# Kernel optimization log

Measured on AMD Instinct MI355X. Metric: run time of the kernel, lower is better.

Reference implementation:

```python
import jax, jax.numpy as jnp
import numpy as np

# dims matching init_kwargs
B, C, T = 64, 8, 2048
K, DIL = 16, 4            # kernel_size, dilation
MLP = 16                  # mlp_dim
NF = min(MLP, K // 2 + 1) # n_frequencies = 9
FEAT = C * NF * 2         # 144
H1, H2 = 64, 32           # ReLUBlock hidden dims (64 -> 64//2)
EFF = DIL * (K - 1)       # 60
W = T - EFF               # 1988 windows


def setup_inputs() -> dict:
    key = jax.random.key(0)
    ks = jax.random.split(key, 10)
    def lin(k, out_d, in_d):
        kw, kb = jax.random.split(k)
        bound = 1.0 / np.sqrt(in_d)
        w = jax.random.uniform(kw, (out_d, in_d), jnp.float32, -bound, bound)
        b = jax.random.uniform(kb, (out_d,), jnp.float32, -bound, bound)
        return w, b
    x = jax.random.normal(ks[0], (B, C, T), jnp.float32)
    proj_w, proj_b = lin(ks[1], MLP, FEAT)
    w1, b1 = lin(ks[2], H1, MLP)
    w2, b2 = lin(ks[3], H2, H1)
    out_w, out_b = lin(ks[4], 1, H2)
    agg_w = jax.random.normal(ks[5], (W,), jnp.float32) * 0.1
    return {"x": x, "proj_w": proj_w, "proj_b": proj_b, "w1": w1, "b1": b1,
            "w2": w2, "b2": b2, "out_w": out_w, "out_b": out_b, "agg_w": agg_w}


def reference(x, proj_w, proj_b, w1, b1, w2, b2, out_w, out_b, agg_w):
    # Build all dilated windows at once: window[t, j] = x[..., t - (K-1-j)*DIL]
    starts = jnp.arange(EFF, T)                      # [W]
    offs = -(K - 1 - jnp.arange(K)) * DIL            # [K]
    idx = starts[:, None] + offs[None, :]            # [W, K]
    win = x[:, :, idx]                               # [B, C, W, K]
    f = jnp.fft.rfft(win, axis=-1)[..., :NF]         # [B, C, W, NF]
    mag = jnp.log1p(jnp.abs(f))
    ph = jnp.angle(f) / jnp.pi
    feat = jnp.stack([mag, ph], axis=-1)             # [B, C, W, NF, 2]
    feat = feat.transpose(0, 2, 1, 3, 4).reshape(B, W, FEAT)  # [B, W, C*NF*2]
    p = jnp.tanh(feat @ proj_w.T + proj_b) * jnp.pi  # [B, W, MLP]
    h = jax.nn.relu(p @ w1.T + b1)                   # [B, W, H1]
    h = jax.nn.relu(h @ w2.T + b2)                   # [B, W, H2]
    out = (h @ out_w.T + out_b)[..., 0]              # [B, W]
    wts = jax.nn.softmax(agg_w)                      # [W]
    return (out * wts[None, :]).sum(axis=1)          # [B]
```

## Files before the change

### kernel.cpp

```cpp
#include <hip/hip_runtime.h>
#include <math.h>

#define B_    64
#define C_    8
#define T_    2048
#define K_    16
#define NF_   9
#define FEAT_ 144
#define MLP_  16
#define H1_   64
#define H2_   32
#define EFF_  60
#define W_    1988
#define NCHK_ 32
#define PI_F  3.14159265358979323846f
#define SPW   36
#define S1    20
#define S2    36

typedef float v2f __attribute__((ext_vector_type(2)));
__device__ __forceinline__ void pkfma(v2f& acc, v2f a, v2f b) {
  asm("v_pk_fma_f32 %0, %1, %2, %0" : "+v"(acc) : "v"(a), "v"(b));
}
__device__ __forceinline__ v2f mkv2(float x, float y) { v2f r; r.x = x; r.y = y; return r; }
__device__ __forceinline__ v2f lo2(float4 a) { return mkv2(a.x, a.y); }
__device__ __forceinline__ v2f hi2(float4 a) { return mkv2(a.z, a.w); }

constexpr float COS16[16] = {
   1.0f,  0.92387953251128674f,  0.70710678118654752f,  0.38268343236508977f,
   0.0f, -0.38268343236508977f, -0.70710678118654752f, -0.92387953251128674f,
  -1.0f, -0.92387953251128674f, -0.70710678118654752f, -0.38268343236508977f,
   0.0f,  0.38268343236508977f,  0.70710678118654752f,  0.92387953251128674f };
constexpr float SIN16F[16] = {
   0.0f,  0.38268343236508977f,  0.70710678118654752f,  0.92387953251128674f,
   1.0f,  0.92387953251128674f,  0.70710678118654752f,  0.38268343236508977f,
   0.0f, -0.38268343236508977f, -0.70710678118654752f, -0.92387953251128674f,
  -1.0f, -0.92387953251128674f, -0.70710678118654752f, -0.38268343236508977f };

__device__ __forceinline__ float fast_log1p(float s) {
  return __builtin_amdgcn_logf(1.0f + s) * 0.69314718055994531f;
}
__device__ __forceinline__ float atanpi_poly(float r) {
  const float s2 = r * r;
  float p = -0.0037310f;
  p = fmaf(p, s2,  0.0167600f);
  p = fmaf(p, s2, -0.0370617f);
  p = fmaf(p, s2,  0.0616068f);
  p = fmaf(p, s2, -0.10587734f);
  p = fmaf(p, s2,  0.31830265f);
  return r * p;
}
__device__ __forceinline__ float atan2pi_fast(float im, float re) {
  const float ax = fabsf(re), ay = fabsf(im);
  const float mx = fmaxf(ax, ay), mn = fminf(ax, ay);
  const float r = mn * __builtin_amdgcn_rcpf(fmaxf(mx, 1e-37f));
  float t = atanpi_poly(r);
  t = (ay > ax) ? 0.5f - t : t;
  t = (__float_as_uint(re) & 0x80000000u) ? 1.0f - t : t;
  return copysignf(t, im);
}
__device__ __forceinline__ float fast_tanh(float z) {
  const float az = fabsf(z);
  const float e = __builtin_amdgcn_exp2f(-2.8853900817779268f * az);
  const float th = fmaf(-2.0f, e * __builtin_amdgcn_rcpf(1.0f + e), 1.0f);
  return copysignf(th, z);
}

__global__ __launch_bounds__(256) void setup_kernel(const float* __restrict__ agg,
                                                    float* __restrict__ wts,
                                                    const float* __restrict__ pw,
                                                    const float* __restrict__ w2,
                                                    float* __restrict__ PWt,
                                                    float* __restrict__ W2t) {
  if (blockIdx.x == 0) {
    __shared__ float red[256];
    const int tid = threadIdx.x;
    float m = -INFINITY;
    for (int i = tid; i < W_; i += 256) m = fmaxf(m, agg[i]);
    red[tid] = m; __syncthreads();
    for (int s = 128; s > 0; s >>= 1) { if (tid < s) red[tid] = fmaxf(red[tid], red[tid+s]); __syncthreads(); }
    const float mx = red[0];
    __syncthreads();
    float sum = 0.f;
    for (int i = tid; i < W_; i += 256) sum += expf(agg[i] - mx);
    red[tid] = sum; __syncthreads();
    for (int s = 128; s > 0; s >>= 1) { if (tid < s) red[tid] += red[tid+s]; __syncthreads(); }
    const float inv = 1.f / red[0];
    for (int i = tid; i < W_; i += 256) wts[i] = expf(agg[i] - mx) * inv;
  } else {
    const int tid = (blockIdx.x - 1) * 256 + threadIdx.x;
    if (tid < MLP_ * FEAT_) {
      const int j = tid / FEAT_, f = tid - j * FEAT_;
      PWt[f * MLP_ + j] = pw[tid];
    }
    if (tid < H2_ * H1_) {
      const int m = tid >> 6, i = tid & 63;
      W2t[i * H2_ + m] = w2[tid];
    }
  }
}

__global__ __launch_bounds__(256) void tcn_fused(
    const float* __restrict__ x,
    const float* __restrict__ PWt, const float* __restrict__ proj_b,
    const float* __restrict__ w1, const float* __restrict__ b1,
    const float* __restrict__ W2t, const float* __restrict__ b2,
    const float* __restrict__ out_w, const float* __restrict__ out_b,
    const float* __restrict__ wts, float* __restrict__ partials) {
  __shared__ __align__(16) float PWl[72 * SPW];
  __shared__ __align__(16) float W1p[H1_ * S1];
  __shared__ __align__(16) float W2p[H1_ * S2];
  __shared__ float B1s[H1_];

  const int tid = threadIdx.x;
  for (int idx = tid; idx < 72 * 32; idx += 256) { const int r = idx >> 5, j = idx & 31; PWl[r * SPW + j] = PWt[idx]; }
  for (int idx = tid; idx < H1_ * MLP_; idx += 256) { const int i = idx >> 4, j = idx & 15; W1p[i * S1 + j] = w1[idx]; }
  for (int idx = tid; idx < H1_ * H2_; idx += 256) { const int i = idx >> 5, m = idx & 31; W2p[i * S2 + m] = W2t[idx]; }
  if (tid < H1_) B1s[tid] = b1[tid];
  __syncthreads();

  const int lane = tid & 63;
  const int wave = tid >> 6;
  const int wloc = lane & 15;
  const int sub  = lane >> 4;
  const int b     = blockIdx.y;
  const int chunk = blockIdx.x;
  const int w  = chunk * 64 + wave * 16 + wloc;
  const int wl = (w < W_) ? w : (W_ - 1);

  v2f pacc2[8];
  #pragma unroll
  for (int q = 0; q < 8; q++) pacc2[q] = mkv2(0.f, 0.f);

  #pragma unroll
  for (int cc = 0; cc < 2; cc++) {
    const int c = sub * 2 + cc;
    const float* xc = x + ((size_t)b * C_ + c) * T_ + wl;
    float win[K_];
    #pragma unroll
    for (int k = 0; k < K_; k++) win[k] = xc[k * 4];
    float ae[8], bo[8];
    #pragma unroll
    for (int k = 0; k < 8; k++) { ae[k] = win[k] + win[k+8]; bo[k] = win[k] - win[k+8]; }

    {
      const float r0 = ((ae[0]+ae[1])+(ae[2]+ae[3]))+((ae[4]+ae[5])+(ae[6]+ae[7]));
      const float r8 = ((ae[0]-ae[1])+(ae[2]-ae[3]))+((ae[4]-ae[5])+(ae[6]-ae[7]));
      const float mag0 = fast_log1p(fabsf(r0));
      const float mag8 = fast_log1p(fabsf(r8));
      const float ph0 = (__float_as_uint(r0) >> 31) ? 1.f : 0.f;
      const float ph8 = (__float_as_uint(r8) >> 31) ? 1.f : 0.f;
      const float4* rv0 = reinterpret_cast<const float4*>(&PWl[(c * NF_ + 0) * SPW]);
      const float4* rv8 = reinterpret_cast<const float4*>(&PWl[(c * NF_ + 8) * SPW]);
      const v2f mm0 = mkv2(mag0, mag0), pp0 = mkv2(ph0, ph0);
      const v2f mm8 = mkv2(mag8, mag8), pp8 = mkv2(ph8, ph8);
      #pragma unroll
      for (int q = 0; q < 4; q++) {
        const float4 a0 = rv0[q], c0 = rv0[q + 4];
        const float4 a8 = rv8[q], c8 = rv8[q + 4];
        pkfma(pacc2[2*q],   mm0, lo2(a0));  pkfma(pacc2[2*q],   pp0, lo2(c0));
        pkfma(pacc2[2*q+1], mm0, hi2(a0));  pkfma(pacc2[2*q+1], pp0, hi2(c0));
        pkfma(pacc2[2*q],   mm8, lo2(a8));  pkfma(pacc2[2*q],   pp8, lo2(c8));
        pkfma(pacc2[2*q+1], mm8, hi2(a8));  pkfma(pacc2[2*q+1], pp8, hi2(c8));
      }
    }

    #pragma unroll
    for (int n = 1; n < 8; n++) {
      float re = 0.f, im = 0.f;
      #pragma unroll
      for (int k = 0; k < 8; k++) {
        const float v = (n & 1) ? bo[k] : ae[k];
        const int t = (n * k) & 15;
        re = fmaf(v,  COS16[t],  re);
        im = fmaf(v, -SIN16F[t], im);
      }
      const float s   = __builtin_amdgcn_sqrtf(fmaf(re, re, im * im));
      const float mag = fast_log1p(s);
      const float ph  = atan2pi_fast(im, re);
      const float4* rmv = reinterpret_cast<const float4*>(&PWl[(c * NF_ + n) * SPW]);
      const v2f mm = mkv2(mag, mag), pp = mkv2(ph, ph);
      #pragma unroll
      for (int q = 0; q < 4; q++) {
        const float4 a  = rmv[q];
        const float4 bb = rmv[q + 4];
        pkfma(pacc2[2*q],   mm, lo2(a));  pkfma(pacc2[2*q],   pp, lo2(bb));
        pkfma(pacc2[2*q+1], mm, hi2(a));  pkfma(pacc2[2*q+1], pp, hi2(bb));
      }
    }
  }

  float* pf = reinterpret_cast<float*>(pacc2);
  #pragma unroll
  for (int j = 0; j < MLP_; j++) {
    pf[j] += __shfl_xor(pf[j], 16, 64);
    pf[j] += __shfl_xor(pf[j], 32, 64);
  }
  v2f p2[8];
  #pragma unroll
  for (int q = 0; q < 8; q++) {
    p2[q] = mkv2(fast_tanh(pf[2*q]   + proj_b[2*q])   * PI_F,
                 fast_tanh(pf[2*q+1] + proj_b[2*q+1]) * PI_F);
  }

  v2f h2a2[16];
  #pragma unroll
  for (int q = 0; q < 16; q++) h2a2[q] = mkv2(0.f, 0.f);
  #pragma unroll 4
  for (int ii = 0; ii < 16; ii++) {
    const int i = sub + ii * 4;
    const float4* r1 = reinterpret_cast<const float4*>(&W1p[i * S1]);
    v2f acc2 = mkv2(B1s[i], 0.f);
    #pragma unroll
    for (int q = 0; q < 4; q++) {
      const float4 a = r1[q];
      pkfma(acc2, p2[2*q],   lo2(a));
      pkfma(acc2, p2[2*q+1], hi2(a));
    }
    const float h1v = fmaxf(acc2.x + acc2.y, 0.f);
    const v2f hh = mkv2(h1v, h1v);
    const float4* r2 = reinterpret_cast<const float4*>(&W2p[i * S2]);
    #pragma unroll
    for (int q = 0; q < 8; q++) {
      const float4 a = r2[q];
      pkfma(h2a2[2*q],   hh, lo2(a));
      pkfma(h2a2[2*q+1], hh, hi2(a));
    }
  }
  float* hf = reinterpret_cast<float*>(h2a2);
  #pragma unroll
  for (int m = 0; m < H2_; m++) {
    hf[m] += __shfl_xor(hf[m], 16, 64);
    hf[m] += __shfl_xor(hf[m], 32, 64);
  }

  float o = 0.f;
  #pragma unroll
  for (int t = 0; t < 8; t++) {
    const int m = sub * 8 + t;
    o = fmaf(fmaxf(hf[m] + b2[m], 0.f), out_w[m], o);
  }
  o += __shfl_xor(o, 16, 64);
  o += __shfl_xor(o, 32, 64);
  o += out_b[0];

  float val = (sub == 0 && w < W_) ? o * wts[wl] : 0.f;
  #pragma unroll
  for (int s = 1; s < 16; s <<= 1) val += __shfl_xor(val, s, 64);
  if (lane == 0) partials[(b * NCHK_ + chunk) * 4 + wave] = val;
}

__global__ void finalize_kernel(const float* __restrict__ partials, float* __restrict__ out) {
  const int b = threadIdx.x;
  if (b < B_) {
    float s = 0.f;
    #pragma unroll 4
    for (int c = 0; c < NCHK_ * 4; c++) s += partials[b * NCHK_ * 4 + c];
    out[b] = s;
  }
}

extern "C" void kernel_launch(void* const* d_in, const int* in_sizes, int n_in,
                              void* d_out, int out_size, void* d_ws, size_t ws_size,
                              hipStream_t stream) {
  const float* x      = (const float*)d_in[0];
  const float* proj_w = (const float*)d_in[1];
  const float* proj_b = (const float*)d_in[2];
  const float* w1     = (const float*)d_in[3];
  const float* b1     = (const float*)d_in[4];
  const float* w2     = (const float*)d_in[5];
  const float* b2     = (const float*)d_in[6];
  const float* out_w  = (const float*)d_in[7];
  const float* out_b  = (const float*)d_in[8];
  const float* agg_w  = (const float*)d_in[9];

  float* wts      = (float*)d_ws;
  float* PWt      = (float*)d_ws + 2048;
  float* W2t      = (float*)d_ws + 2048 + 2304;
  float* partials = (float*)d_ws + 8192;

  setup_kernel<<<10, 256, 0, stream>>>(agg_w, wts, proj_w, w2, PWt, W2t);
  tcn_fused<<<dim3(NCHK_, B_), 256, 0, stream>>>(x, PWt, proj_b, w1, b1, W2t, b2,
                                                 out_w, out_b, wts, partials);
  finalize_kernel<<<1, 64, 0, stream>>>(partials, (float*)d_out);
}
```

Before: 58.02 us.

## Process two windows per thread and parallelize finalize reduction across blocks

Each thread now handles two windows 64 apart, halving the grid (NCHK 32→16). The shared-memory weight reads, the one-time block setup and the weight staging are amortized over two windows, and the doubled independent work gives more ILP. The finalize kernel changes from one thread per batch summing serially to one 64-lane block per batch reducing with shuffles. The cost is much higher register pressure, which may reduce occupancy, and fewer blocks in flight.

```diff
diff --git a/kernel.cpp b/kernel.cpp
--- a/kernel.cpp
+++ b/kernel.cpp
@@ -12,7 +12,7 @@
 #define H2_   32
 #define EFF_  60
 #define W_    1988
-#define NCHK_ 32
+#define NCHK_ 16
 #define PI_F  3.14159265358979323846f
 #define SPW   36
 #define S1    20
@@ -125,139 +125,183 @@
   const int sub  = lane >> 4;
   const int b     = blockIdx.y;
   const int chunk = blockIdx.x;
-  const int w  = chunk * 64 + wave * 16 + wloc;
-  const int wl = (w < W_) ? w : (W_ - 1);
-
-  v2f pacc2[8];
-  #pragma unroll
-  for (int q = 0; q < 8; q++) pacc2[q] = mkv2(0.f, 0.f);
+  const int wA = chunk * 128 + wave * 16 + wloc;
+  const int wB = wA + 64;
+  const int wBl = (wB < W_) ? wB : (W_ - 1);
+
+  v2f paccA[8], paccB[8];
+  #pragma unroll
+  for (int q = 0; q < 8; q++) { paccA[q] = mkv2(0.f, 0.f); paccB[q] = mkv2(0.f, 0.f); }
 
   #pragma unroll
   for (int cc = 0; cc < 2; cc++) {
     const int c = sub * 2 + cc;
-    const float* xc = x + ((size_t)b * C_ + c) * T_ + wl;
-    float win[K_];
-    #pragma unroll
-    for (int k = 0; k < K_; k++) win[k] = xc[k * 4];
-    float ae[8], bo[8];
-    #pragma unroll
-    for (int k = 0; k < 8; k++) { ae[k] = win[k] + win[k+8]; bo[k] = win[k] - win[k+8]; }
+    const float* xrow = x + ((size_t)b * C_ + c) * T_;
+    const float* xcA = xrow + wA;
+    const float* xcB = xrow + wBl;
+    float winA[K_], winB[K_];
+    #pragma unroll
+    for (int k = 0; k < K_; k++) { winA[k] = xcA[k * 4]; winB[k] = xcB[k * 4]; }
+    float aeA[8], boA[8], aeB[8], boB[8];
+    #pragma unroll
+    for (int k = 0; k < 8; k++) {
+      aeA[k] = winA[k] + winA[k+8]; boA[k] = winA[k] - winA[k+8];
+      aeB[k] = winB[k] + winB[k+8]; boB[k] = winB[k] - winB[k+8];
+    }
 
     {
-      const float r0 = ((ae[0]+ae[1])+(ae[2]+ae[3]))+((ae[4]+ae[5])+(ae[6]+ae[7]));
-      const float r8 = ((ae[0]-ae[1])+(ae[2]-ae[3]))+((ae[4]-ae[5])+(ae[6]-ae[7]));
-      const float mag0 = fast_log1p(fabsf(r0));
-      const float mag8 = fast_log1p(fabsf(r8));
-      const float ph0 = (__float_as_uint(r0) >> 31) ? 1.f : 0.f;
-      const float ph8 = (__float_as_uint(r8) >> 31) ? 1.f : 0.f;
+      const float r0A = ((aeA[0]+aeA[1])+(aeA[2]+aeA[3]))+((aeA[4]+aeA[5])+(aeA[6]+aeA[7]));
+      const float r8A = ((aeA[0]-aeA[1])+(aeA[2]-aeA[3]))+((aeA[4]-aeA[5])+(aeA[6]-aeA[7]));
+      const float r0B = ((aeB[0]+aeB[1])+(aeB[2]+aeB[3]))+((aeB[4]+aeB[5])+(aeB[6]+aeB[7]));
+      const float r8B = ((aeB[0]-aeB[1])+(aeB[2]-aeB[3]))+((aeB[4]-aeB[5])+(aeB[6]-aeB[7]));
+      const float m0A = fast_log1p(fabsf(r0A)), m8A = fast_log1p(fabsf(r8A));
+      const float m0B = fast_log1p(fabsf(r0B)), m8B = fast_log1p(fabsf(r8B));
+      const float p0A = (__float_as_uint(r0A) >> 31) ? 1.f : 0.f;
+      const float p8A = (__float_as_uint(r8A) >> 31) ? 1.f : 0.f;
+      const float p0B = (__float_as_uint(r0B) >> 31) ? 1.f : 0.f;
+      const float p8B = (__float_as_uint(r8B) >> 31) ? 1.f : 0.f;
+      const v2f mm0A = mkv2(m0A, m0A), mm8A = mkv2(m8A, m8A);
+      const v2f mm0B = mkv2(m0B, m0B), mm8B = mkv2(m8B, m8B);
+      const v2f pp0A = mkv2(p0A, p0A), pp8A = mkv2(p8A, p8A);
+      const v2f pp0B = mkv2(p0B, p0B), pp8B = mkv2(p8B, p8B);
       const float4* rv0 = reinterpret_cast<const float4*>(&PWl[(c * NF_ + 0) * SPW]);
       const float4* rv8 = reinterpret_cast<const float4*>(&PWl[(c * NF_ + 8) * SPW]);
-      const v2f mm0 = mkv2(mag0, mag0), pp0 = mkv2(ph0, ph0);
-      const v2f mm8 = mkv2(mag8, mag8), pp8 = mkv2(ph8, ph8);
       #pragma unroll
       for (int q = 0; q < 4; q++) {
         const float4 a0 = rv0[q], c0 = rv0[q + 4];
         const float4 a8 = rv8[q], c8 = rv8[q + 4];
-        pkfma(pacc2[2*q],   mm0, lo2(a0));  pkfma(pacc2[2*q],   pp0, lo2(c0));
-        pkfma(pacc2[2*q+1], mm0, hi2(a0));  pkfma(pacc2[2*q+1], pp0, hi2(c0));
-        pkfma(pacc2[2*q],   mm8, lo2(a8));  pkfma(pacc2[2*q],   pp8, lo2(c8));
-        pkfma(pacc2[2*q+1], mm8, hi2(a8));  pkfma(pacc2[2*q+1], pp8, hi2(c8));
+        pkfma(paccA[2*q],   mm0A, lo2(a0));  pkfma(paccA[2*q],   pp0A, lo2(c0));
+        pkfma(paccA[2*q+1], mm0A, hi2(a0));  pkfma(paccA[2*q+1], pp0A, hi2(c0));
+        pkfma(paccA[2*q],   mm8A, lo2(a8));  pkfma(paccA[2*q],   pp8A, lo2(c8));
+        pkfma(paccA[2*q+1], mm8A, hi2(a8));  pkfma(paccA[2*q+1], pp8A, hi2(c8));
+        pkfma(paccB[2*q],   mm0B, lo2(a0));  pkfma(paccB[2*q],   pp0B, lo2(c0));
+        pkfma(paccB[2*q+1], mm0B, hi2(a0));  pkfma(paccB[2*q+1], pp0B, hi2(c0));
+        pkfma(paccB[2*q],   mm8B, lo2(a8));  pkfma(paccB[2*q],   pp8B, lo2(c8));
+        pkfma(paccB[2*q+1], mm8B, hi2(a8));  pkfma(paccB[2*q+1], pp8B, hi2(c8));
       }
     }
 
     #pragma unroll
     for (int n = 1; n < 8; n++) {
-      float re = 0.f, im = 0.f;
+      float reA = 0.f, imA = 0.f, reB = 0.f, imB = 0.f;
       #pragma unroll
       for (int k = 0; k < 8; k++) {
-        const float v = (n & 1) ? bo[k] : ae[k];
         const int t = (n * k) & 15;
-        re = fmaf(v,  COS16[t],  re);
-        im = fmaf(v, -SIN16F[t], im);
+        const float cv = COS16[t], sv = -SIN16F[t];
+        const float vA = (n & 1) ? boA[k] : aeA[k];
+        const float vB = (n & 1) ? boB[k] : aeB[k];
+        reA = fmaf(vA, cv, reA); imA = fmaf(vA, sv, imA);
+        reB = fmaf(vB, cv, reB); imB = fmaf(vB, sv, imB);
       }
-      const float s   = __builtin_amdgcn_sqrtf(fmaf(re, re, im * im));
-      const float mag = fast_log1p(s);
-      const float ph  = atan2pi_fast(im, re);
+      const float sA = __builtin_amdgcn_sqrtf(fmaf(reA, reA, imA * imA));
+      const float sB = __builtin_amdgcn_sqrtf(fmaf(reB, reB, imB * imB));
+      const float magA = fast_log1p(sA), magB = fast_log1p(sB);
+      const float phA = atan2pi_fast(imA, reA), phB = atan2pi_fast(imB, reB);
+      const v2f mmA = mkv2(magA, magA), ppA = mkv2(phA, phA);
+      const v2f mmB = mkv2(magB, magB), ppB = mkv2(phB, phB);
       const float4* rmv = reinterpret_cast<const float4*>(&PWl[(c * NF_ + n) * SPW]);
-      const v2f mm = mkv2(mag, mag), pp = mkv2(ph, ph);
       #pragma unroll
       for (int q = 0; q < 4; q++) {
         const float4 a  = rmv[q];
         const float4 bb = rmv[q + 4];
-        pkfma(pacc2[2*q],   mm, lo2(a));  pkfma(pacc2[2*q],   pp, lo2(bb));
-        pkfma(pacc2[2*q+1], mm, hi2(a));  pkfma(pacc2[2*q+1], pp, hi2(bb));
+        pkfma(paccA[2*q],   mmA, lo2(a));  pkfma(paccA[2*q],   ppA, lo2(bb));
+        pkfma(paccA[2*q+1], mmA, hi2(a));  pkfma(paccA[2*q+1], ppA, hi2(bb));
+        pkfma(paccB[2*q],   mmB, lo2(a));  pkfma(paccB[2*q],   ppB, lo2(bb));
+        pkfma(paccB[2*q+1], mmB, hi2(a));  pkfma(paccB[2*q+1], ppB, hi2(bb));
       }
     }
   }
 
-  float* pf = reinterpret_cast<float*>(pacc2);
+  float* pfA = reinterpret_cast<float*>(paccA);
+  float* pfB = reinterpret_cast<float*>(paccB);
   #pragma unroll
   for (int j = 0; j < MLP_; j++) {
-    pf[j] += __shfl_xor(pf[j], 16, 64);
-    pf[j] += __shfl_xor(pf[j], 32, 64);
-  }
-  v2f p2[8];
+    pfA[j] += __shfl_xor(pfA[j], 16, 64);
+    pfA[j] += __shfl_xor(pfA[j], 32, 64);
+    pfB[j] += __shfl_xor(pfB[j], 16, 64);
+    pfB[j] += __shfl_xor(pfB[j], 32, 64);
+  }
+  v2f p2A[8], p2B[8];
   #pragma unroll
   for (int q = 0; q < 8; q++) {
-    p2[q] = mkv2(fast_tanh(pf[2*q]   + proj_b[2*q])   * PI_F,
-                 fast_tanh(pf[2*q+1] + proj_b[2*q+1]) * PI_F);
-  }
-
-  v2f h2a2[16];
-  #pragma unroll
-  for (int q = 0; q < 16; q++) h2a2[q] = mkv2(0.f, 0.f);
+    p2A[q] = mkv2(fast_tanh(pfA[2*q]   + proj_b[2*q])   * PI_F,
+                  fast_tanh(pfA[2*q+1] + proj_b[2*q+1]) * PI_F);
+    p2B[q] = mkv2(fast_tanh(pfB[2*q]   + proj_b[2*q])   * PI_F,
+                  fast_tanh(pfB[2*q+1] + proj_b[2*q+1]) * PI_F);
+  }
+
+  v2f h2aA[16], h2aB[16];
+  #pragma unroll
+  for (int q = 0; q < 16; q++) { h2aA[q] = mkv2(0.f, 0.f); h2aB[q] = mkv2(0.f, 0.f); }
   #pragma unroll 4
   for (int ii = 0; ii < 16; ii++) {
     const int i = sub + ii * 4;
     const float4* r1 = reinterpret_cast<const float4*>(&W1p[i * S1]);
-    v2f acc2 = mkv2(B1s[i], 0.f);
+    v2f accA = mkv2(B1s[i], 0.f), accB = mkv2(B1s[i], 0.f);
     #pragma unroll
     for (int q = 0; q < 4; q++) {
       const float4 a = r1[q];
-      pkfma(acc2, p2[2*q],   lo2(a));
-      pkfma(acc2, p2[2*q+1], hi2(a));
-    }
-    const float h1v = fmaxf(acc2.x + acc2.y, 0.f);
-    const v2f hh = mkv2(h1v, h1v);
+      pkfma(accA, p2A[2*q],   lo2(a));
+      pkfma(accA, p2A[2*q+1], hi2(a));
+      pkfma(accB, p2B[2*q],   lo2(a));
+      pkfma(accB, p2B[2*q+1], hi2(a));
+    }
+    const float h1A = fmaxf(accA.x + accA.y, 0.f);
+    const float h1B = fmaxf(accB.x + accB.y, 0.f);
+    const v2f hhA = mkv2(h1A, h1A), hhB = mkv2(h1B, h1B);
     const float4* r2 = reinterpret_cast<const float4*>(&W2p[i * S2]);
     #pragma unroll
     for (int q = 0; q < 8; q++) {
       const float4 a = r2[q];
-      pkfma(h2a2[2*q],   hh, lo2(a));
-      pkfma(h2a2[2*q+1], hh, hi2(a));
-    }
-  }
-  float* hf = reinterpret_cast<float*>(h2a2);
+      pkfma(h2aA[2*q],   hhA, lo2(a));
+      pkfma(h2aA[2*q+1], hhA, hi2(a));
+      pkfma(h2aB[2*q],   hhB, lo2(a));
+      pkfma(h2aB[2*q+1], hhB, hi2(a));
+    }
+  }
+  float* hfA = reinterpret_cast<float*>(h2aA);
+  float* hfB = reinterpret_cast<float*>(h2aB);
   #pragma unroll
   for (int m = 0; m < H2_; m++) {
-    hf[m] += __shfl_xor(hf[m], 16, 64);
-    hf[m] += __shfl_xor(hf[m], 32, 64);
-  }
-
-  float o = 0.f;
+    hfA[m] += __shfl_xor(hfA[m], 16, 64);
+    hfA[m] += __shfl_xor(hfA[m], 32, 64);
+    hfB[m] += __shfl_xor(hfB[m], 16, 64);
+    hfB[m] += __shfl_xor(hfB[m], 32, 64);
+  }
+
+  float oA = 0.f, oB = 0.f;
   #pragma unroll
   for (int t = 0; t < 8; t++) {
     const int m = sub * 8 + t;
-    o = fmaf(fmaxf(hf[m] + b2[m], 0.f), out_w[m], o);
-  }
-  o += __shfl_xor(o, 16, 64);
-  o += __shfl_xor(o, 32, 64);
-  o += out_b[0];
-
-  float val = (sub == 0 && w < W_) ? o * wts[wl] : 0.f;
+    const float bm = b2[m], wm = out_w[m];
+    oA = fmaf(fmaxf(hfA[m] + bm, 0.f), wm, oA);
+    oB = fmaf(fmaxf(hfB[m] + bm, 0.f), wm, oB);
+  }
+  oA += __shfl_xor(oA, 16, 64);
+  oA += __shfl_xor(oA, 32, 64);
+  oA += out_b[0];
+  oB += __shfl_xor(oB, 16, 64);
+  oB += __shfl_xor(oB, 32, 64);
+  oB += out_b[0];
+
+  float val = 0.f;
+  if (sub == 0) {
+    val = oA * wts[wA];
+    if (wB < W_) val = fmaf(oB, wts[wB], val);
+  }
   #pragma unroll
   for (int s = 1; s < 16; s <<= 1) val += __shfl_xor(val, s, 64);
   if (lane == 0) partials[(b * NCHK_ + chunk) * 4 + wave] = val;
 }
 
-__global__ void finalize_kernel(const float* __restrict__ partials, float* __restrict__ out) {
-  const int b = threadIdx.x;
-  if (b < B_) {
-    float s = 0.f;
-    #pragma unroll 4
-    for (int c = 0; c < NCHK_ * 4; c++) s += partials[b * NCHK_ * 4 + c];
-    out[b] = s;
-  }
+__global__ __launch_bounds__(64) void finalize_kernel(const float* __restrict__ partials,
+                                                      float* __restrict__ out) {
+  const int b = blockIdx.x;
+  const int l = threadIdx.x;
+  float s = partials[b * NCHK_ * 4 + l];
+  #pragma unroll
+  for (int d = 1; d < 64; d <<= 1) s += __shfl_xor(s, d, 64);
+  if (l == 0) out[b] = s;
 }
 
 extern "C" void kernel_launch(void* const* d_in, const int* in_sizes, int n_in,
@@ -282,5 +326,5 @@
   setup_kernel<<<10, 256, 0, stream>>>(agg_w, wts, proj_w, w2, PWt, W2t);
   tcn_fused<<<dim3(NCHK_, B_), 256, 0, stream>>>(x, PWt, proj_b, w1, b1, W2t, b2,
                                                  out_w, out_b, wts, partials);
-  finalize_kernel<<<1, 64, 0, stream>>>(partials, (float*)d_out);
-}
+  finalize_kernel<<<B_, 64, 0, stream>>>(partials, (float*)d_out);
+}
```

After: 53.99 us (median of 2 runs). 1.07x faster.
